# Performance work log

Measured on AMD Instinct MI355X. Metric: run time of the kernel, lower is better.

## Reference

```python
import jax, jax.numpy as jnp
import numpy as np

B, V, D, NH, DH = 1, 6, 256, 8, 32
L, ZP = 4, 4
BEV = 80
Q = BEV * BEV
SHAPES = [(56, 100), (28, 50), (14, 25), (7, 13)]
N = sum(h * w for h, w in SHAPES)
PAD_H, PAD_W = 448, 800
PC = (-48.0, -48.0, -5.0, 48.0, 48.0, 3.0)
EPS = 1e-5


def _ref3d():
    # get_reference_points + pc_range scaling; the original overwrites the z channel
    # with scaled-x (code bug: ref_3d[...,2:3] = ref_3d[...,:1]*zrange+zmin) -> reproduced faithfully,
    # so all ZP pillar points are identical.
    u = jnp.arange(Q)
    xs = ((u % BEV).astype(jnp.float32) + 0.5) / BEV
    ys = ((u // BEV).astype(jnp.float32) + 0.5) / BEV
    x = xs * (PC[3] - PC[0]) + PC[0]
    y = ys * (PC[4] - PC[1]) + PC[1]
    z = x * (PC[5] - PC[2]) + PC[2]
    p = jnp.stack([x, y, z], -1)  # [Q,3]
    return jnp.broadcast_to(p[None], (ZP, Q, 3))


def _project(l2i):
    # l2i: [B,V,4,4] -> normalized coords [B,V,Q,ZP,2], validity mask [B,V,Q,ZP]
    pts = _ref3d().reshape(-1, 3)
    pts_h = jnp.concatenate([pts, jnp.ones_like(pts[:, :1])], -1)  # [ZP*Q,4]
    ip = jnp.einsum('bvij,nj->bvni', l2i, pts_h)                   # [B,V,ZP*Q,4]
    zc = ip[..., 2]
    xy = ip[..., :2] / jnp.clip(zc, EPS, None)[..., None]
    xn = xy[..., 0] / PAD_W
    yn = xy[..., 1] / PAD_H
    m = (zc > EPS) & (xn > 0) & (xn < 1) & (yn > 0) & (yn < 1)
    coords = jnp.stack([xn, yn], -1).reshape(B, V, ZP, Q, 2).transpose(0, 1, 3, 2, 4)
    mask = m.reshape(B, V, ZP, Q).transpose(0, 1, 3, 2)
    return coords, mask


def _forward(feat0, feat1, feat2, feat3, lidar2img_mat, bev_emb, level_embeds,
             view_embeds, value_W, value_b, off_W, off_b, aw_W, aw_b, out_W, out_b):
    feats = [feat0, feat1, feat2, feat3]
    parts = []
    for l, f in enumerate(feats):
        h, w = SHAPES[l]
        x = f.reshape(B, V, D, h * w).transpose(0, 1, 3, 2)  # [B,V,hw,D]
        x = x + view_embeds[None, :, None, :] + level_embeds[l]
        parts.append(x)
    feat_flat = jnp.concatenate(parts, axis=2)  # [B,V,N,D]

    coords, mask = _project(lidar2img_mat)
    mask_any = mask.any(-1)                                            # [B,V,Q]
    count = jnp.clip(mask_any.sum(1).astype(jnp.float32), 1.0, None)   # [B,Q]

    value = (feat_flat.reshape(B * V, N, D) @ value_W + value_b).reshape(B * V, N, NH, DH)
    off = (bev_emb @ off_W + off_b).reshape(Q, NH, L, ZP, 2)
    aw = jax.nn.softmax((bev_emb @ aw_W + aw_b).reshape(Q, NH, L * ZP), -1).reshape(Q, NH, L, ZP)
    ref = coords.reshape(B * V, Q, ZP, 2)

    out = jnp.zeros((B * V, Q, NH, DH), feat_flat.dtype)
    start = 0
    for l, (h, w) in enumerate(SHAPES):
        v_l = value[:, start:start + h * w].transpose(0, 2, 1, 3).reshape(B * V * NH, h * w, DH)
        start += h * w
        loc = ref[:, :, None, :, :] + off[None, :, :, l] / jnp.array([w, h], feat_flat.dtype)
        loc = loc.transpose(0, 2, 1, 3, 4).reshape(B * V * NH, Q * ZP, 2)
        # grid_sample(align_corners=False, padding='zeros') with grid 2*loc-1
        gx = loc[..., 0] * w - 0.5
        gy = loc[..., 1] * h - 0.5
        x0 = jnp.floor(gx).astype(jnp.int32)
        y0 = jnp.floor(gy).astype(jnp.int32)
        wx1 = gx - x0
        wy1 = gy - y0

        def corner(xi, yi, wt):
            valid = (xi >= 0) & (xi < w) & (yi >= 0) & (yi < h)
            lin = jnp.clip(yi, 0, h - 1) * w + jnp.clip(xi, 0, w - 1)
            g = jnp.take_along_axis(v_l, lin[..., None], axis=1)
            return g * (wt * valid)[..., None]

        s = (corner(x0, y0, (1 - wx1) * (1 - wy1)) + corner(x0 + 1, y0, wx1 * (1 - wy1))
             + corner(x0, y0 + 1, (1 - wx1) * wy1) + corner(x0 + 1, y0 + 1, wx1 * wy1))
        s = s.reshape(B * V, NH, Q, ZP, DH)
        out = out + jnp.einsum('vhqzd,qhz->vqhd', s, aw[:, :, l])

    attn = out.reshape(B, V, Q, D)
    slots = (attn * mask_any[..., None]).sum(1) / count[..., None]
    slots = slots @ out_W + out_b
    return bev_emb[None] + slots  # dropout is identity at inference


def setup_inputs() -> dict:
    key = jax.random.key(0)
    ks = jax.random.split(key, 16)
    s = 0.02
    return {
        'feat0': jax.random.normal(ks[0], (B, V, D) + SHAPES[0], jnp.float32),
        'feat1': jax.random.normal(ks[1], (B, V, D) + SHAPES[1], jnp.float32),
        'feat2': jax.random.normal(ks[2], (B, V, D) + SHAPES[2], jnp.float32),
        'feat3': jax.random.normal(ks[3], (B, V, D) + SHAPES[3], jnp.float32),
        'lidar2img_mat': jax.random.normal(ks[4], (B, V, 4, 4), jnp.float32) * 50.0,
        'bev_emb': jax.random.normal(ks[5], (Q, D), jnp.float32) * s,
        'level_embeds': jax.random.normal(ks[6], (L, D), jnp.float32) * s,
        'view_embeds': jax.random.normal(ks[7], (V, D), jnp.float32) * s,
        'value_W': jax.random.normal(ks[8], (D, D), jnp.float32) * s,
        'value_b': jnp.zeros((D,), jnp.float32),
        'off_W': jax.random.normal(ks[9], (D, NH * L * ZP * 2), jnp.float32) * s,
        'off_b': jnp.zeros((NH * L * ZP * 2,), jnp.float32),
        'aw_W': jax.random.normal(ks[10], (D, NH * L * ZP), jnp.float32) * s,
        'aw_b': jnp.zeros((NH * L * ZP,), jnp.float32),
        'out_W': jax.random.normal(ks[11], (D, D), jnp.float32) * s,
        'out_b': jnp.zeros((D,), jnp.float32),
    }


def reference(feat0, feat1, feat2, feat3, lidar2img_mat, bev_emb, level_embeds,
              view_embeds, value_W, value_b, off_W, off_b, aw_W, aw_b, out_W, out_b):
    return _forward(feat0, feat1, feat2, feat3, lidar2img_mat, bev_emb, level_embeds,
                    view_embeds, value_W, value_b, off_W, off_b, aw_W, aw_b, out_W, out_b)
```

## Files before the change

### kernel.cpp

```cpp
#include <hip/hip_runtime.h>
#include <cstdint>
#include <cstddef>

#define NV 6
#define ND 256
#define NHEAD 8
#define NBEV 80
#define NQ 6400
#define NTOK 7441
#define MROWS (NV * NTOK)
#define MROWSP 44672
#define FEPS 1e-5f

#define VBLKS 698
#define GBLKS 848
#define GCHUNK (GBLKS / 8)

#define PR_PROJ 150
#define PR_TR   2832
#define PR_BEV  800
#define PB0 PR_PROJ
#define PB1 (PB0 + PR_TR)
#define PB2 (PB1 + PR_BEV)
#define PB3 (PB2 + 256)
#define PB4 (PB3 + 256)
#define PB5 (PB4 + 128)
#define PB6 (PB5 + 256)
#define PBT (PB6 + 24)

typedef __attribute__((ext_vector_type(8))) short bfx8;
typedef __attribute__((ext_vector_type(4))) float fx4;
typedef __attribute__((ext_vector_type(4))) _Float16 hx4;
typedef __attribute__((ext_vector_type(4))) unsigned short usx4;

__device__ __forceinline__ unsigned short f2bf(float x) {
    uint32_t u = __builtin_bit_cast(uint32_t, x);
    u += 0x7FFFu + ((u >> 16) & 1u);
    return (unsigned short)(u >> 16);
}
__device__ __forceinline__ float lof(uint32_t u) {
    return __builtin_bit_cast(float, u << 16);
}
__device__ __forceinline__ float hif(uint32_t u) {
    return __builtin_bit_cast(float, u & 0xFFFF0000u);
}

__global__ __launch_bounds__(256) void k_prep(
        const float* __restrict__ f0, const float* __restrict__ f1,
        const float* __restrict__ f2, const float* __restrict__ f3,
        const float* __restrict__ l2i, const float* __restrict__ bev,
        const float* __restrict__ ve, const float* __restrict__ le,
        const float* __restrict__ vW, const float* __restrict__ vB,
        const float* __restrict__ oW, const float* __restrict__ aW,
        const float* __restrict__ outW,
        float2* __restrict__ coords, int* __restrict__ mask,
        unsigned short* __restrict__ featT, unsigned short* __restrict__ bevh,
        unsigned short* __restrict__ vWt, unsigned short* __restrict__ oaWt,
        unsigned short* __restrict__ outWt, float* __restrict__ emb_proj) {
    int bid = blockIdx.x;
    int t = threadIdx.x;
    if (bid < PB0) {
        int idx = bid * 256 + t;
        int v = idx / NQ, q = idx - v * NQ;
        float xs = ((float)(q % NBEV) + 0.5f) / (float)NBEV;
        float ys = ((float)(q / NBEV) + 0.5f) / (float)NBEV;
        float x = xs * 96.0f - 48.0f;
        float y = ys * 96.0f - 48.0f;
        float z = x * 8.0f - 5.0f;
        const float* M = l2i + v * 16;
        float ip0 = M[0] * x + M[1] * y + M[2] * z + M[3];
        float ip1 = M[4] * x + M[5] * y + M[6] * z + M[7];
        float ip2 = M[8] * x + M[9] * y + M[10] * z + M[11];
        float dz = fmaxf(ip2, FEPS);
        float xn = ip0 / dz / 800.0f;
        float yn = ip1 / dz / 448.0f;
        bool m = (ip2 > FEPS) && (xn > 0.0f) && (xn < 1.0f) && (yn > 0.0f) && (yn < 1.0f);
        coords[idx] = make_float2(xn, yn);
        mask[idx] = m ? 1 : 0;
    } else if (bid < PB1) {
        __shared__ float T[64][65];
        int idx = bid - PB0;
        int v = idx / 472;
        int rem = idx - v * 472;
        int mt = rem >> 2, kt = rem & 3;
        int hw, p0, st;
        const float* base;
        if (mt < 88)       { base = f0; hw = 5600; st = 0;    p0 = mt * 64; }
        else if (mt < 110) { base = f1; hw = 1400; st = 5600; p0 = (mt - 88) * 64; }
        else if (mt < 116) { base = f2; hw = 350;  st = 7000; p0 = (mt - 110) * 64; }
        else               { base = f3; hw = 91;   st = 7350; p0 = (mt - 116) * 64; }
        int k0 = kt * 64;
        const float* src = base + (size_t)v * 256 * hw;
#pragma unroll
        for (int i = 0; i < 16; ++i) {
            int ii = t + i * 256;
            int kk = ii >> 6, mm = ii & 63;
            float val = (p0 + mm < hw) ? src[(size_t)(k0 + kk) * hw + p0 + mm] : 0.0f;
            T[kk][mm] = val;
        }
        __syncthreads();
#pragma unroll
        for (int i = 0; i < 16; ++i) {
            int ii = t + i * 256;
            int mm = ii >> 6, kk = ii & 63;
            if (p0 + mm < hw)
                featT[(size_t)(v * NTOK + st + p0 + mm) * 256 + k0 + kk] = f2bf(T[kk][mm]);
        }
    } else if (bid < PB2) {
        size_t e = (size_t)(bid - PB1) * 2048 + t * 8;
        float4 a = *(const float4*)(bev + e);
        float4 b = *(const float4*)(bev + e + 4);
        bfx8 o;
        o[0] = (short)f2bf(a.x); o[1] = (short)f2bf(a.y);
        o[2] = (short)f2bf(a.z); o[3] = (short)f2bf(a.w);
        o[4] = (short)f2bf(b.x); o[5] = (short)f2bf(b.y);
        o[6] = (short)f2bf(b.z); o[7] = (short)f2bf(b.w);
        *(bfx8*)(bevh + e) = o;
    } else if (bid < PB3) {
        int e = (bid - PB2) * 256 + t;
        int k = e >> 8, n = e & 255;
        vWt[(size_t)n * 256 + k] = f2bf(vW[(size_t)k * 256 + n]);
    } else if (bid < PB4) {
        int e = (bid - PB3) * 256 + t;
        int k = e >> 8, n = e & 255;
        oaWt[(size_t)n * 256 + k] = f2bf(oW[(size_t)k * 256 + n]);
    } else if (bid < PB5) {
        int e = (bid - PB4) * 256 + t;
        int k = e >> 7, n = e & 127;
        oaWt[(size_t)(256 + n) * 256 + k] = f2bf(aW[(size_t)k * 128 + n]);
    } else if (bid < PB6) {
        int e = (bid - PB5) * 256 + t;
        int k = e >> 8, n = e & 255;
        outWt[(size_t)n * 256 + k] = f2bf(outW[(size_t)k * 256 + n]);
    } else {
        int blk = bid - PB6;
        int v = blk >> 2, l = blk & 3;
        float acc = vB[t];
        for (int d = 0; d < ND; ++d)
            acc += (ve[v * ND + d] + le[l * ND + d]) * vW[d * ND + t];
        emb_proj[blk * ND + t] = acc;
    }
}

__global__ __launch_bounds__(256) void k_gemms(
        const unsigned short* __restrict__ featT,
        const unsigned short* __restrict__ vWt, const float* __restrict__ emb_proj,
        unsigned short* __restrict__ value,
        const unsigned short* __restrict__ bevh,
        const unsigned short* __restrict__ oaWt,
        const float* __restrict__ oB, const float* __restrict__ aB,
        float* __restrict__ off, float* __restrict__ aw_pre) {
    __shared__ unsigned short As[128][72];
    __shared__ unsigned short Bs[128][72];
    int b = blockIdx.x;
    int lb = (b & 7) * GCHUNK + (b >> 3);
    int t = threadIdx.x;
    int lane = t & 63, w = t >> 6;
    int wm = w >> 1, wn = w & 1;
    int lr = lane & 15, lk = lane >> 4;

    bool isval = lb < VBLKS;
    int m0, c0;
    const unsigned short *ap, *bp;
    if (isval) {
        m0 = (lb >> 1) * 128; c0 = (lb & 1) * 128;
        ap = featT; bp = vWt;
    } else {
        int r6 = lb - VBLKS;
        m0 = (r6 / 3) * 128; c0 = (r6 % 3) * 128;
        ap = bevh; bp = oaWt;
    }
    int sr = t >> 1, sk = (t & 1) * 32;
    const unsigned short* arow = ap + (size_t)(m0 + sr) * 256 + sk;
    const unsigned short* brow = bp + (size_t)(c0 + sr) * 256 + sk;

    fx4 acc[4][4];
#pragma unroll
    for (int i = 0; i < 4; ++i)
#pragma unroll
        for (int j = 0; j < 4; ++j) acc[i][j] = (fx4)0.0f;

    for (int k0 = 0; k0 < 256; k0 += 64) {
        bfx8 a0 = *(const bfx8*)(arow + k0);
        bfx8 a1 = *(const bfx8*)(arow + k0 + 8);
        bfx8 a2 = *(const bfx8*)(arow + k0 + 16);
        bfx8 a3 = *(const bfx8*)(arow + k0 + 24);
        bfx8 b0 = *(const bfx8*)(brow + k0);
        bfx8 b1 = *(const bfx8*)(brow + k0 + 8);
        bfx8 b2 = *(const bfx8*)(brow + k0 + 16);
        bfx8 b3 = *(const bfx8*)(brow + k0 + 24);
        *(bfx8*)&As[sr][sk]      = a0;
        *(bfx8*)&As[sr][sk + 8]  = a1;
        *(bfx8*)&As[sr][sk + 16] = a2;
        *(bfx8*)&As[sr][sk + 24] = a3;
        *(bfx8*)&Bs[sr][sk]      = b0;
        *(bfx8*)&Bs[sr][sk + 8]  = b1;
        *(bfx8*)&Bs[sr][sk + 16] = b2;
        *(bfx8*)&Bs[sr][sk + 24] = b3;
        __syncthreads();
#pragma unroll
        for (int ks = 0; ks < 64; ks += 32) {
            bfx8 af[4], bf[4];
#pragma unroll
            for (int f = 0; f < 4; ++f) {
                af[f] = *(bfx8*)&As[wm * 64 + f * 16 + lr][ks + lk * 8];
                bf[f] = *(bfx8*)&Bs[wn * 64 + f * 16 + lr][ks + lk * 8];
            }
#pragma unroll
            for (int fm = 0; fm < 4; ++fm)
#pragma unroll
                for (int fn = 0; fn < 4; ++fn)
                    acc[fm][fn] = __builtin_amdgcn_mfma_f32_16x16x32_bf16(
                        af[fm], bf[fn], acc[fm][fn], 0, 0, 0);
        }
        __syncthreads();
    }

    if (isval) {
#pragma unroll
        for (int fm = 0; fm < 4; ++fm) {
#pragma unroll
            for (int r = 0; r < 4; ++r) {
                int m = m0 + wm * 64 + fm * 16 + lk * 4 + r;
                if (m >= MROWS) continue;
                int v = m / NTOK;
                int n = m - v * NTOK;
                int l = (n < 5600) ? 0 : (n < 7000) ? 1 : (n < 7350) ? 2 : 3;
                const float* ep = emb_proj + (size_t)(v * 4 + l) * ND;
#pragma unroll
                for (int fn = 0; fn < 4; ++fn) {
                    int col = c0 + wn * 64 + fn * 16 + lr;
                    value[(size_t)m * ND + col] = f2bf(acc[fm][fn][r] + ep[col]);
                }
            }
        }
    } else if (c0 < 256) {
#pragma unroll
        for (int fm = 0; fm < 4; ++fm) {
#pragma unroll
            for (int fn = 0; fn < 4; ++fn) {
                int col = c0 + wn * 64 + fn * 16 + lr;
                float bs = oB[col];
#pragma unroll
                for (int r = 0; r < 4; ++r) {
                    int m = m0 + wm * 64 + fm * 16 + lk * 4 + r;
                    off[(size_t)m * 256 + col] = acc[fm][fn][r] + bs;
                }
            }
        }
    } else {
#pragma unroll
        for (int fm = 0; fm < 4; ++fm) {
#pragma unroll
            for (int fn = 0; fn < 4; ++fn) {
                int col = wn * 64 + fn * 16 + lr;
                float bs = aB[col];
#pragma unroll
                for (int r = 0; r < 4; ++r) {
                    int m = m0 + wm * 64 + fm * 16 + lk * 4 + r;
                    aw_pre[(size_t)m * 128 + col] = acc[fm][fn][r] + bs;
                }
            }
        }
    }
}

#define SQB 2
__global__ __launch_bounds__(256) void k_sample(
        const float2* __restrict__ coords, const int* __restrict__ mask,
        const float* __restrict__ off, const float* __restrict__ awlog,
        const unsigned short* __restrict__ value, float* __restrict__ slots) {
    __shared__ float aw_s[SQB][128];
    __shared__ unsigned short lin_s[SQB][NV][128][4];
    __shared__ _Float16 w_s[SQB][NV][128][4];
    __shared__ float2 cxy_s[SQB][NV];
    __shared__ int msk_s[SQB][NV];

    int b = blockIdx.x;
    int lb = (b & 7) * (NQ / SQB / 8) + (b >> 3);
    int q0 = lb * SQB;
    int t = threadIdx.x;
    if (t < SQB * NV) {
        int qq = t / NV, v = t - qq * NV;
        msk_s[qq][v] = mask[v * NQ + q0 + qq];
        cxy_s[qq][v] = coords[v * NQ + q0 + qq];
    }
    {
        int qq = t >> 7, c2 = t & 127;
        aw_s[qq][c2] = awlog[(size_t)(q0 + qq) * 128 + c2];
    }
    __syncthreads();
    if (t < SQB * NHEAD) {
        int qq = t >> 3, h = t & 7;
        float* p = &aw_s[qq][h * 16];
        float mx = p[0];
#pragma unroll
        for (int i = 1; i < 16; ++i) mx = fmaxf(mx, p[i]);
        float e[16];
        float s = 0.0f;
#pragma unroll
        for (int i = 0; i < 16; ++i) { e[i] = __expf(p[i] - mx); s += e[i]; }
        float inv = 1.0f / s;
#pragma unroll
        for (int i = 0; i < 16; ++i) p[i] = e[i] * inv;
    }
    __syncthreads();

    const int LW[4] = {100, 50, 25, 13};
    const int LH[4] = {56, 28, 14, 7};
    const int LST[4] = {0, 5600, 7000, 7350};
    for (int idx = t; idx < SQB * NV * 128; idx += 256) {
        int c2 = idx & 127;
        int rem = idx >> 7;
        int qq = rem / NV, v = rem - qq * NV;
        if (!msk_s[qq][v]) continue;
        int ll = (c2 >> 2) & 3;
        int iwl = LW[ll], ihl = LH[ll], st = LST[ll];
        float wl = (float)iwl, hl = (float)ihl;
        float2 o2 = *(const float2*)&off[(size_t)(q0 + qq) * 256 + 2 * c2];
        float2 cc = cxy_s[qq][v];
        float gx = cc.x * wl + o2.x - 0.5f;
        float gy = cc.y * hl + o2.y - 0.5f;
        float fxf = floorf(gx), fyf = floorf(gy);
        int x0 = (int)fxf, y0 = (int)fyf;
        float wx = gx - fxf, wy = gy - fyf;
        bool bx0 = (unsigned)x0 < (unsigned)iwl;
        bool bx1 = (unsigned)(x0 + 1) < (unsigned)iwl;
        bool by0 = (unsigned)y0 < (unsigned)ihl;
        bool by1 = (unsigned)(y0 + 1) < (unsigned)ihl;
        int cx0 = min(max(x0, 0), iwl - 1);
        int cx1 = min(max(x0 + 1, 0), iwl - 1);
        int cy0 = min(max(y0, 0), ihl - 1);
        int cy1 = min(max(y0 + 1, 0), ihl - 1);
        float wa = aw_s[qq][c2];
        int r0 = st + cy0 * iwl, r1 = st + cy1 * iwl;
        usx4 lin;
        lin.x = (unsigned short)(r0 + cx0);
        lin.y = (unsigned short)(r0 + cx1);
        lin.z = (unsigned short)(r1 + cx0);
        lin.w = (unsigned short)(r1 + cx1);
        hx4 ww;
        ww.x = (_Float16)((bx0 && by0) ? (1.0f - wx) * (1.0f - wy) * wa : 0.0f);
        ww.y = (_Float16)((bx1 && by0) ? wx * (1.0f - wy) * wa : 0.0f);
        ww.z = (_Float16)((bx0 && by1) ? (1.0f - wx) * wy * wa : 0.0f);
        ww.w = (_Float16)((bx1 && by1) ? wx * wy * wa : 0.0f);
        *(usx4*)lin_s[qq][v][c2] = lin;
        *(hx4*)w_s[qq][v][c2] = ww;
    }
    __syncthreads();

    int qq = t >> 7, cp = t & 127;
    int hb = (cp >> 4) * 16;
    float acc0 = 0.0f, acc1 = 0.0f;
    int cnt = 0;
#pragma unroll
    for (int v = 0; v < NV; ++v) cnt += msk_s[qq][v];
    for (int v = 0; v < NV; ++v) {
        if (!msk_s[qq][v]) continue;
        const uint32_t* vb = (const uint32_t*)(value + (size_t)v * NTOK * 256) + cp;
#pragma unroll
        for (int ci = 0; ci < 16; ++ci) {
            int c2 = hb + ci;
            usx4 lin = *(const usx4*)lin_s[qq][v][c2];
            hx4 wh = *(const hx4*)w_s[qq][v][c2];
            uint32_t u0 = vb[(size_t)lin.x * 128];
            uint32_t u1 = vb[(size_t)lin.y * 128];
            uint32_t u2 = vb[(size_t)lin.z * 128];
            uint32_t u3 = vb[(size_t)lin.w * 128];
            float w0 = (float)wh.x, w1 = (float)wh.y;
            float w2 = (float)wh.z, w3 = (float)wh.w;
            acc0 += w0 * lof(u0) + w1 * lof(u1) + w2 * lof(u2) + w3 * lof(u3);
            acc1 += w0 * hif(u0) + w1 * hif(u1) + w2 * hif(u2) + w3 * hif(u3);
        }
    }
    float invc = 1.0f / fmaxf((float)cnt, 1.0f);
    *(float2*)&slots[(size_t)(q0 + qq) * 256 + 2 * cp] = make_float2(acc0 * invc, acc1 * invc);
}

__global__ __launch_bounds__(256) void k_out(
        const float* __restrict__ A, const unsigned short* __restrict__ Bt,
        const float* __restrict__ bias, const float* __restrict__ addsrc,
        float* __restrict__ out) {
    __shared__ unsigned short As[64][40];
    __shared__ unsigned short Bs[128][40];
    int t = threadIdx.x;
    int m0 = blockIdx.x * 64, c0 = blockIdx.y * 128;
    int lane = t & 63, w = t >> 6;
    int wm = w >> 1, wn = w & 1;
    int lr = lane & 15, lk = lane >> 4;
    int mA = t & 63, kg = t >> 6;
    const float* ap = A + (size_t)(m0 + mA) * 256 + kg * 8;
    const unsigned short* bp = Bt + (size_t)(c0 + (t >> 1)) * 256 + (t & 1) * 16;
    fx4 acc[2][4];
#pragma unroll
    for (int i = 0; i < 2; ++i)
#pragma unroll
        for (int j = 0; j < 4; ++j) acc[i][j] = (fx4)0.0f;
    for (int k0 = 0; k0 < 256; k0 += 32) {
        float va[8];
        *(float4*)&va[0] = *(const float4*)(ap + k0);
        *(float4*)&va[4] = *(const float4*)(ap + k0 + 4);
        bfx8 a8;
#pragma unroll
        for (int i = 0; i < 8; ++i) a8[i] = (short)f2bf(va[i]);
        *(bfx8*)&As[mA][kg * 8] = a8;
        *(bfx8*)&Bs[t >> 1][(t & 1) * 16] = *(const bfx8*)(bp + k0);
        *(bfx8*)&Bs[t >> 1][(t & 1) * 16 + 8] = *(const bfx8*)(bp + k0 + 8);
        __syncthreads();
        bfx8 af[2], bf[4];
#pragma unroll
        for (int f = 0; f < 2; ++f)
            af[f] = *(bfx8*)&As[wm * 32 + f * 16 + lr][lk * 8];
#pragma unroll
        for (int f = 0; f < 4; ++f)
            bf[f] = *(bfx8*)&Bs[wn * 64 + f * 16 + lr][lk * 8];
#pragma unroll
        for (int fm = 0; fm < 2; ++fm)
#pragma unroll
            for (int fn = 0; fn < 4; ++fn)
                acc[fm][fn] = __builtin_amdgcn_mfma_f32_16x16x32_bf16(
                    af[fm], bf[fn], acc[fm][fn], 0, 0, 0);
        __syncthreads();
    }
#pragma unroll
    for (int fm = 0; fm < 2; ++fm) {
#pragma unroll
        for (int fn = 0; fn < 4; ++fn) {
            int col = c0 + wn * 64 + fn * 16 + lr;
            float bs = bias[col];
#pragma unroll
            for (int r = 0; r < 4; ++r) {
                int m = m0 + wm * 32 + fm * 16 + lk * 4 + r;
                out[(size_t)m * 256 + col] =
                    acc[fm][fn][r] + bs + addsrc[(size_t)m * 256 + col];
            }
        }
    }
}

extern "C" void kernel_launch(void* const* d_in, const int* in_sizes, int n_in,
                              void* d_out, int out_size, void* d_ws, size_t ws_size,
                              hipStream_t stream) {
    const float* f0   = (const float*)d_in[0];
    const float* f1   = (const float*)d_in[1];
    const float* f2   = (const float*)d_in[2];
    const float* f3   = (const float*)d_in[3];
    const float* l2i  = (const float*)d_in[4];
    const float* bev  = (const float*)d_in[5];
    const float* le   = (const float*)d_in[6];
    const float* ve   = (const float*)d_in[7];
    const float* vW   = (const float*)d_in[8];
    const float* vB   = (const float*)d_in[9];
    const float* oW   = (const float*)d_in[10];
    const float* oB   = (const float*)d_in[11];
    const float* aW   = (const float*)d_in[12];
    const float* aB   = (const float*)d_in[13];
    const float* outW = (const float*)d_in[14];
    const float* outB = (const float*)d_in[15];
    float* out = (float*)d_out;

    char* ws = (char*)d_ws;
    size_t o = 0;
    auto alloc = [&](size_t bytes) {
        void* p = ws + o;
        o += (bytes + 255) & ~(size_t)255;
        return p;
    };
    float2* coords   = (float2*)alloc((size_t)NV * NQ * sizeof(float2));
    int*    mask     = (int*)alloc((size_t)NV * NQ * sizeof(int));
    float*  emb_proj = (float*)alloc((size_t)24 * ND * sizeof(float));
    float*  off      = (float*)alloc((size_t)NQ * 256 * sizeof(float));
    float*  aw_pre   = (float*)alloc((size_t)NQ * 128 * sizeof(float));
    float*  slots    = (float*)alloc((size_t)NQ * 256 * sizeof(float));
    unsigned short* value = (unsigned short*)alloc((size_t)MROWS * ND * sizeof(short));
    unsigned short* featT = (unsigned short*)alloc((size_t)MROWSP * ND * sizeof(short));
    unsigned short* bevh  = (unsigned short*)alloc((size_t)NQ * ND * sizeof(short));
    unsigned short* vWt   = (unsigned short*)alloc((size_t)256 * 256 * sizeof(short));
    unsigned short* oaWt  = (unsigned short*)alloc((size_t)384 * 256 * sizeof(short));
    unsigned short* outWt = (unsigned short*)alloc((size_t)256 * 256 * sizeof(short));

    k_prep<<<PBT, 256, 0, stream>>>(f0, f1, f2, f3, l2i, bev, ve, le, vW, vB,
                                    oW, aW, outW, coords, mask, featT, bevh,
                                    vWt, oaWt, outWt, emb_proj);
    k_gemms<<<GBLKS, 256, 0, stream>>>(featT, vWt, emb_proj, value,
                                       bevh, oaWt, oB, aB, off, aw_pre);
    k_sample<<<NQ / SQB, 256, 0, stream>>>(coords, mask, off, aw_pre, value, slots);
    dim3 gout(NQ / 64, 2);
    k_out<<<gout, 256, 0, stream>>>(slots, outWt, outB, bev, out);
}
```

Baseline: 186.7 us.

## Prefetch global tiles into registers in GEMMs, vectorize transposes, pack sampling metadata

Both MFMA GEMM kernels now load the next K-slice from global memory into registers while the current slice is being computed, with the K-step cut to 32 and smaller LDS tiles. The feature transpose in the prep kernel writes 8 bf16 values per thread as one 16-byte store instead of scalar stores. The sampling kernel packs its four bilinear indices and four fp16 weights into one uint4 per entry in shared memory, so each entry is one 16-byte LDS read. The intent is to hide global load latency and cut memory instruction counts. The cost is higher register pressure and twice as many barriers in the value GEMM.

```diff
diff --git a/kernel.cpp b/kernel.cpp
--- a/kernel.cpp
+++ b/kernel.cpp
@@ -30,8 +30,6 @@
 
 typedef __attribute__((ext_vector_type(8))) short bfx8;
 typedef __attribute__((ext_vector_type(4))) float fx4;
-typedef __attribute__((ext_vector_type(4))) _Float16 hx4;
-typedef __attribute__((ext_vector_type(4))) unsigned short usx4;
 
 __device__ __forceinline__ unsigned short f2bf(float x) {
     uint32_t u = __builtin_bit_cast(uint32_t, x);
@@ -43,6 +41,12 @@
 }
 __device__ __forceinline__ float hif(uint32_t u) {
     return __builtin_bit_cast(float, u & 0xFFFF0000u);
+}
+__device__ __forceinline__ unsigned short f2h(float x) {
+    return __builtin_bit_cast(unsigned short, (_Float16)x);
+}
+__device__ __forceinline__ float h2f(unsigned short h) {
+    return (float)__builtin_bit_cast(_Float16, h);
 }
 
 __global__ __launch_bounds__(256) void k_prep(
@@ -99,12 +103,18 @@
             T[kk][mm] = val;
         }
         __syncthreads();
-#pragma unroll
-        for (int i = 0; i < 16; ++i) {
-            int ii = t + i * 256;
-            int mm = ii >> 6, kk = ii & 63;
-            if (p0 + mm < hw)
-                featT[(size_t)(v * NTOK + st + p0 + mm) * 256 + k0 + kk] = f2bf(T[kk][mm]);
+        size_t row0 = (size_t)v * NTOK + st + p0;
+        int slot = t & 7;
+#pragma unroll
+        for (int j = 0; j < 2; ++j) {
+            int mm = (t >> 3) + j * 32;
+            if (p0 + mm < hw) {
+                bfx8 o;
+#pragma unroll
+                for (int jj = 0; jj < 8; ++jj)
+                    o[jj] = (short)f2bf(T[slot * 8 + jj][mm]);
+                *(bfx8*)&featT[(row0 + mm) * 256 + k0 + slot * 8] = o;
+            }
         }
     } else if (bid < PB2) {
         size_t e = (size_t)(bid - PB1) * 2048 + t * 8;
@@ -150,8 +160,8 @@
         const unsigned short* __restrict__ oaWt,
         const float* __restrict__ oB, const float* __restrict__ aB,
         float* __restrict__ off, float* __restrict__ aw_pre) {
-    __shared__ unsigned short As[128][72];
-    __shared__ unsigned short Bs[128][72];
+    __shared__ unsigned short As[128][40];
+    __shared__ unsigned short Bs[128][40];
     int b = blockIdx.x;
     int lb = (b & 7) * GCHUNK + (b >> 3);
     int t = threadIdx.x;
@@ -170,9 +180,9 @@
         m0 = (r6 / 3) * 128; c0 = (r6 % 3) * 128;
         ap = bevh; bp = oaWt;
     }
-    int sr = t >> 1, sk = (t & 1) * 32;
-    const unsigned short* arow = ap + (size_t)(m0 + sr) * 256 + sk;
-    const unsigned short* brow = bp + (size_t)(c0 + sr) * 256 + sk;
+    int sr = t & 127, skh = (t >> 7) * 16;
+    const unsigned short* arow = ap + (size_t)(m0 + sr) * 256 + skh;
+    const unsigned short* brow = bp + (size_t)(c0 + sr) * 256 + skh;
 
     fx4 acc[4][4];
 #pragma unroll
@@ -180,38 +190,34 @@
 #pragma unroll
         for (int j = 0; j < 4; ++j) acc[i][j] = (fx4)0.0f;
 
-    for (int k0 = 0; k0 < 256; k0 += 64) {
-        bfx8 a0 = *(const bfx8*)(arow + k0);
-        bfx8 a1 = *(const bfx8*)(arow + k0 + 8);
-        bfx8 a2 = *(const bfx8*)(arow + k0 + 16);
-        bfx8 a3 = *(const bfx8*)(arow + k0 + 24);
-        bfx8 b0 = *(const bfx8*)(brow + k0);
-        bfx8 b1 = *(const bfx8*)(brow + k0 + 8);
-        bfx8 b2 = *(const bfx8*)(brow + k0 + 16);
-        bfx8 b3 = *(const bfx8*)(brow + k0 + 24);
-        *(bfx8*)&As[sr][sk]      = a0;
-        *(bfx8*)&As[sr][sk + 8]  = a1;
-        *(bfx8*)&As[sr][sk + 16] = a2;
-        *(bfx8*)&As[sr][sk + 24] = a3;
-        *(bfx8*)&Bs[sr][sk]      = b0;
-        *(bfx8*)&Bs[sr][sk + 8]  = b1;
-        *(bfx8*)&Bs[sr][sk + 16] = b2;
-        *(bfx8*)&Bs[sr][sk + 24] = b3;
+    bfx8 ar0 = *(const bfx8*)arow;
+    bfx8 ar1 = *(const bfx8*)(arow + 8);
+    bfx8 br0 = *(const bfx8*)brow;
+    bfx8 br1 = *(const bfx8*)(brow + 8);
+#pragma unroll
+    for (int k0 = 0; k0 < 256; k0 += 32) {
+        *(bfx8*)&As[sr][skh]     = ar0;
+        *(bfx8*)&As[sr][skh + 8] = ar1;
+        *(bfx8*)&Bs[sr][skh]     = br0;
+        *(bfx8*)&Bs[sr][skh + 8] = br1;
         __syncthreads();
-#pragma unroll
-        for (int ks = 0; ks < 64; ks += 32) {
-            bfx8 af[4], bf[4];
-#pragma unroll
-            for (int f = 0; f < 4; ++f) {
-                af[f] = *(bfx8*)&As[wm * 64 + f * 16 + lr][ks + lk * 8];
-                bf[f] = *(bfx8*)&Bs[wn * 64 + f * 16 + lr][ks + lk * 8];
-            }
-#pragma unroll
-            for (int fm = 0; fm < 4; ++fm)
-#pragma unroll
-                for (int fn = 0; fn < 4; ++fn)
-                    acc[fm][fn] = __builtin_amdgcn_mfma_f32_16x16x32_bf16(
-                        af[fm], bf[fn], acc[fm][fn], 0, 0, 0);
+        if (k0 < 224) {
+            ar0 = *(const bfx8*)(arow + k0 + 32);
+            ar1 = *(const bfx8*)(arow + k0 + 40);
+            br0 = *(const bfx8*)(brow + k0 + 32);
+            br1 = *(const bfx8*)(brow + k0 + 40);
+        }
+        bfx8 bfv[4];
+#pragma unroll
+        for (int f = 0; f < 4; ++f)
+            bfv[f] = *(bfx8*)&Bs[wn * 64 + f * 16 + lr][lk * 8];
+#pragma unroll
+        for (int fm = 0; fm < 4; ++fm) {
+            bfx8 afv = *(bfx8*)&As[wm * 64 + fm * 16 + lr][lk * 8];
+#pragma unroll
+            for (int fn = 0; fn < 4; ++fn)
+                acc[fm][fn] = __builtin_amdgcn_mfma_f32_16x16x32_bf16(
+                    afv, bfv[fn], acc[fm][fn], 0, 0, 0);
         }
         __syncthreads();
     }
@@ -271,8 +277,7 @@
         const float* __restrict__ off, const float* __restrict__ awlog,
         const unsigned short* __restrict__ value, float* __restrict__ slots) {
     __shared__ float aw_s[SQB][128];
-    __shared__ unsigned short lin_s[SQB][NV][128][4];
-    __shared__ _Float16 w_s[SQB][NV][128][4];
+    __shared__ uint4 lw_s[SQB][NV][128];
     __shared__ float2 cxy_s[SQB][NV];
     __shared__ int msk_s[SQB][NV];
 
@@ -334,18 +339,16 @@
         int cy1 = min(max(y0 + 1, 0), ihl - 1);
         float wa = aw_s[qq][c2];
         int r0 = st + cy0 * iwl, r1 = st + cy1 * iwl;
-        usx4 lin;
-        lin.x = (unsigned short)(r0 + cx0);
-        lin.y = (unsigned short)(r0 + cx1);
-        lin.z = (unsigned short)(r1 + cx0);
-        lin.w = (unsigned short)(r1 + cx1);
-        hx4 ww;
-        ww.x = (_Float16)((bx0 && by0) ? (1.0f - wx) * (1.0f - wy) * wa : 0.0f);
-        ww.y = (_Float16)((bx1 && by0) ? wx * (1.0f - wy) * wa : 0.0f);
-        ww.z = (_Float16)((bx0 && by1) ? (1.0f - wx) * wy * wa : 0.0f);
-        ww.w = (_Float16)((bx1 && by1) ? wx * wy * wa : 0.0f);
-        *(usx4*)lin_s[qq][v][c2] = lin;
-        *(hx4*)w_s[qq][v][c2] = ww;
+        float w00 = (bx0 && by0) ? (1.0f - wx) * (1.0f - wy) * wa : 0.0f;
+        float w01 = (bx1 && by0) ? wx * (1.0f - wy) * wa : 0.0f;
+        float w10 = (bx0 && by1) ? (1.0f - wx) * wy * wa : 0.0f;
+        float w11 = (bx1 && by1) ? wx * wy * wa : 0.0f;
+        uint4 lw;
+        lw.x = (uint32_t)(unsigned short)(r0 + cx0) | ((uint32_t)(unsigned short)(r0 + cx1) << 16);
+        lw.y = (uint32_t)(unsigned short)(r1 + cx0) | ((uint32_t)(unsigned short)(r1 + cx1) << 16);
+        lw.z = (uint32_t)f2h(w00) | ((uint32_t)f2h(w01) << 16);
+        lw.w = (uint32_t)f2h(w10) | ((uint32_t)f2h(w11) << 16);
+        lw_s[qq][v][c2] = lw;
     }
     __syncthreads();
 
@@ -360,15 +363,15 @@
         const uint32_t* vb = (const uint32_t*)(value + (size_t)v * NTOK * 256) + cp;
 #pragma unroll
         for (int ci = 0; ci < 16; ++ci) {
-            int c2 = hb + ci;
-            usx4 lin = *(const usx4*)lin_s[qq][v][c2];
-            hx4 wh = *(const hx4*)w_s[qq][v][c2];
-            uint32_t u0 = vb[(size_t)lin.x * 128];
-            uint32_t u1 = vb[(size_t)lin.y * 128];
-            uint32_t u2 = vb[(size_t)lin.z * 128];
-            uint32_t u3 = vb[(size_t)lin.w * 128];
-            float w0 = (float)wh.x, w1 = (float)wh.y;
-            float w2 = (float)wh.z, w3 = (float)wh.w;
+            uint4 lw = lw_s[qq][v][hb + ci];
+            uint32_t u0 = vb[(size_t)(lw.x & 0xFFFF) * 128];
+            uint32_t u1 = vb[(size_t)(lw.x >> 16) * 128];
+            uint32_t u2 = vb[(size_t)(lw.y & 0xFFFF) * 128];
+            uint32_t u3 = vb[(size_t)(lw.y >> 16) * 128];
+            float w0 = h2f((unsigned short)(lw.z & 0xFFFF));
+            float w1 = h2f((unsigned short)(lw.z >> 16));
+            float w2 = h2f((unsigned short)(lw.w & 0xFFFF));
+            float w3 = h2f((unsigned short)(lw.w >> 16));
             acc0 += w0 * lof(u0) + w1 * lof(u1) + w2 * lof(u2) + w3 * lof(u3);
             acc1 += w0 * hif(u0) + w1 * hif(u1) + w2 * hif(u2) + w3 * hif(u3);
         }
@@ -396,30 +399,40 @@
     for (int i = 0; i < 2; ++i)
 #pragma unroll
         for (int j = 0; j < 4; ++j) acc[i][j] = (fx4)0.0f;
+
+    float4 va0 = *(const float4*)ap;
+    float4 va1 = *(const float4*)(ap + 4);
+    bfx8 brg = *(const bfx8*)bp;
+    bfx8 brg2 = *(const bfx8*)(bp + 8);
+#pragma unroll
     for (int k0 = 0; k0 < 256; k0 += 32) {
-        float va[8];
-        *(float4*)&va[0] = *(const float4*)(ap + k0);
-        *(float4*)&va[4] = *(const float4*)(ap + k0 + 4);
         bfx8 a8;
-#pragma unroll
-        for (int i = 0; i < 8; ++i) a8[i] = (short)f2bf(va[i]);
+        a8[0] = (short)f2bf(va0.x); a8[1] = (short)f2bf(va0.y);
+        a8[2] = (short)f2bf(va0.z); a8[3] = (short)f2bf(va0.w);
+        a8[4] = (short)f2bf(va1.x); a8[5] = (short)f2bf(va1.y);
+        a8[6] = (short)f2bf(va1.z); a8[7] = (short)f2bf(va1.w);
         *(bfx8*)&As[mA][kg * 8] = a8;
-        *(bfx8*)&Bs[t >> 1][(t & 1) * 16] = *(const bfx8*)(bp + k0);
-        *(bfx8*)&Bs[t >> 1][(t & 1) * 16 + 8] = *(const bfx8*)(bp + k0 + 8);
+        *(bfx8*)&Bs[t >> 1][(t & 1) * 16] = brg;
+        *(bfx8*)&Bs[t >> 1][(t & 1) * 16 + 8] = brg2;
         __syncthreads();
-        bfx8 af[2], bf[4];
-#pragma unroll
-        for (int f = 0; f < 2; ++f)
-            af[f] = *(bfx8*)&As[wm * 32 + f * 16 + lr][lk * 8];
+        if (k0 < 224) {
+            va0 = *(const float4*)(ap + k0 + 32);
+            va1 = *(const float4*)(ap + k0 + 36);
+            brg = *(const bfx8*)(bp + k0 + 32);
+            brg2 = *(const bfx8*)(bp + k0 + 40);
+        }
+        bfx8 bfv[4];
 #pragma unroll
         for (int f = 0; f < 4; ++f)
-            bf[f] = *(bfx8*)&Bs[wn * 64 + f * 16 + lr][lk * 8];
-#pragma unroll
-        for (int fm = 0; fm < 2; ++fm)
+            bfv[f] = *(bfx8*)&Bs[wn * 64 + f * 16 + lr][lk * 8];
+#pragma unroll
+        for (int fm = 0; fm < 2; ++fm) {
+            bfx8 afv = *(bfx8*)&As[wm * 32 + fm * 16 + lr][lk * 8];
 #pragma unroll
             for (int fn = 0; fn < 4; ++fn)
                 acc[fm][fn] = __builtin_amdgcn_mfma_f32_16x16x32_bf16(
-                    af[fm], bf[fn], acc[fm][fn], 0, 0, 0);
+                    afv, bfv[fn], acc[fm][fn], 0, 0, 0);
+        }
         __syncthreads();
     }
 #pragma unroll
```

New measurement: 190.4 us. No clear change (+2.0%).
